# Performance work log

Hardware: AMD Instinct MI355X
Metric: run time of the kernel (lower is better)

Reference implementation:

```python
import jax, jax.numpy as jnp
import numpy as np

B, T, C, H, HD = 4, 2048, 1024, 16, 64

def setup_inputs() -> dict:
    key = jax.random.key(0)
    ks = jax.random.split(key, 9)
    s = 1.0 / np.sqrt(C)
    return {
        "x":  jax.random.normal(ks[0], (B, T, C), jnp.float32),
        "Wq": jax.random.normal(ks[1], (H, C, HD), jnp.float32) * s,
        "bq": jax.random.normal(ks[2], (H, HD), jnp.float32) * 0.02,
        "Wk": jax.random.normal(ks[3], (H, C, HD), jnp.float32) * s,
        "bk": jax.random.normal(ks[4], (H, HD), jnp.float32) * 0.02,
        "Wv": jax.random.normal(ks[5], (H, C, HD), jnp.float32) * s,
        "bv": jax.random.normal(ks[6], (H, HD), jnp.float32) * 0.02,
        "Wo": jax.random.normal(ks[7], (C, C), jnp.float32) * s,
        "bo": jax.random.normal(ks[8], (C,), jnp.float32) * 0.02,
    }

def reference(x, Wq, bq, Wk, bk, Wv, bv, Wo, bo):
    # Batched per-head linear projections: [B,T,C] x [H,C,D] -> [B,H,T,D]
    q = jnp.einsum('btc,hcd->bhtd', x, Wq) + bq[None, :, None, :]
    k = jnp.einsum('btc,hcd->bhtd', x, Wk) + bk[None, :, None, :]
    v = jnp.einsum('btc,hcd->bhtd', x, Wv) + bv[None, :, None, :]
    scale = 1.0 / jnp.sqrt(jnp.asarray(HD, q.dtype))
    scores = jnp.einsum('bhtd,bhsd->bhts', q, k) * scale  # [B,H,T,T]
    causal = jnp.tril(jnp.ones((T, T), dtype=bool))
    scores = jnp.where(causal[None, None, :, :], scores, -jnp.inf)
    attn = jax.nn.softmax(scores, axis=-1)
    out = jnp.einsum('bhts,bhsd->bhtd', attn, v)          # [B,H,T,D]
    concat = out.transpose(0, 2, 1, 3).reshape(B, T, C)   # concat heads
    return concat @ Wo + bo
```

## Files before the change

### kernel.cpp

```cpp
#include <hip/hip_runtime.h>
#include <stdint.h>

#define TSEQ 2048
#define NHEAD 16

typedef __attribute__((ext_vector_type(8))) short bf16x8;
typedef __attribute__((ext_vector_type(4))) short bf16x4;
typedef __attribute__((ext_vector_type(4))) float f32x4;

__device__ __forceinline__ unsigned short f2bf(float f) {
  union { float f; uint32_t u; } c;
  c.f = f;
  uint32_t u = c.u;
  u += 0x7fffu + ((u >> 16) & 1u);
  return (unsigned short)(u >> 16);
}

__device__ __forceinline__ float fexp2(float x) {
#if __has_builtin(__builtin_amdgcn_exp2f)
  return __builtin_amdgcn_exp2f(x);
#else
  return __builtin_exp2f(x);
#endif
}

using as3_void  = __attribute__((address_space(3))) void;
using as1_cvoid = const __attribute__((address_space(1))) void;

__device__ __forceinline__ void gld_lds16(const void* g, void* l) {
  __builtin_amdgcn_global_load_lds((as1_cvoid*)g, (as3_void*)l, 16, 0, 0);
}


__global__ void cast_x_kernel(const float4* __restrict__ x, unsigned short* __restrict__ xb) {
  int i = blockIdx.x * 256 + threadIdx.x;
  float4 v = x[i];
  int e = i * 4;
  int m = e >> 10, k = e & 1023;
  int ks = k ^ ((m & 7) << 3);
  ushort4 o;
  o.x = f2bf(v.x); o.y = f2bf(v.y); o.z = f2bf(v.z); o.w = f2bf(v.w);
  *(ushort4*)(xb + (size_t)m * 1024 + ks) = o;
}

__global__ void repack_wqkv(const float* __restrict__ Wq, const float* __restrict__ Wk,
                            const float* __restrict__ Wv, unsigned short* __restrict__ BT) {
  __shared__ unsigned short tile[64][72];
  const float* W = (blockIdx.z == 0) ? Wq : (blockIdx.z == 1) ? Wk : Wv;
  const int h = blockIdx.y;
  const int c0 = blockIdx.x * 64;
  const int t = threadIdx.x;
  const float* src = W + ((size_t)h * 1024 + c0) * 64;
#pragma unroll
  for (int p = 0; p < 16; ++p) {
    int idx = p * 256 + t;
    int cc = idx >> 6, d = idx & 63;
    tile[cc][d] = f2bf(src[(size_t)cc * 64 + d]);
  }
  __syncthreads();
  unsigned short* dst = BT + ((size_t)blockIdx.z * 1024 + (size_t)h * 64) * 1024 + c0;
#pragma unroll
  for (int p = 0; p < 16; ++p) {
    int idx = p * 256 + t;
    int d = idx >> 6, cc = idx & 63;
    dst[(size_t)d * 1024 + (cc ^ ((d & 7) << 3))] = tile[cc][d];
  }
}

__global__ void repack_wo(const float* __restrict__ Wo, unsigned short* __restrict__ WoT) {
  __shared__ unsigned short tile[64][72];
  const int k0 = blockIdx.x * 64;
  const int n0 = blockIdx.y * 64;
  const int t = threadIdx.x;
#pragma unroll
  for (int p = 0; p < 16; ++p) {
    int idx = p * 256 + t;
    int kk = idx >> 6, nn = idx & 63;
    tile[kk][nn] = f2bf(Wo[(size_t)(k0 + kk) * 1024 + n0 + nn]);
  }
  __syncthreads();
#pragma unroll
  for (int p = 0; p < 16; ++p) {
    int idx = p * 256 + t;
    int nn = idx >> 6, kk = idx & 63;
    WoT[(size_t)(n0 + nn) * 1024 + k0 + (kk ^ ((nn & 7) << 3))] = tile[kk][nn];
  }
}


template <int MODE>
__global__ __launch_bounds__(256) void gemm_bt(
    const unsigned short* __restrict__ A, const unsigned short* __restrict__ BTm,
    const float* __restrict__ bias0, const float* __restrict__ bias1,
    const float* __restrict__ bias2,
    unsigned short* __restrict__ qo, unsigned short* __restrict__ ko,
    unsigned short* __restrict__ vto, float* __restrict__ outf,
    int K, int N) {
  __shared__ __align__(16) char lds[65536];

  const int tid = threadIdx.x, lane = tid & 63, wv = tid >> 6;
  const int wr = wv >> 1, wc = wv & 1;
  const int g = lane >> 4, r = lane & 15;
  const int m0 = blockIdx.x * 128, n0 = blockIdx.y * 128;
  const int xr = (r & 7) << 4;

  f32x4 acc[4][4] = {};

  const int arow = tid >> 3;
  const int acol = (tid & 7) * 8;
  const unsigned short* Ab = A + (size_t)(m0 + arow) * K + acol;
  const unsigned short* Bb = BTm + (size_t)(n0 + arow) * K + acol;

#define GSTAGE(b, kel) do {                                                 \
    char* ab_ = lds + (b) * 32768 + wv * 1024;                              \
    _Pragma("unroll") for (int i = 0; i < 4; ++i) {                         \
      gld_lds16(Ab + (size_t)i * 32 * K + (kel), ab_ + i * 4096);           \
      gld_lds16(Bb + (size_t)i * 32 * K + (kel), ab_ + 16384 + i * 4096);   \
    } } while (0)

  const int NT = K >> 6;
  GSTAGE(0, 0);
  __syncthreads();

  for (int t = 0; t < NT; ++t) {
    const int cur = t & 1;
    if (t + 1 < NT) GSTAGE(cur ^ 1, (t + 1) << 6);
    const char* Ar = lds + cur * 32768;
    const char* Br = Ar + 16384;
#pragma unroll
    for (int kk = 0; kk < 2; ++kk) {
      bf16x8 af[4], bfv[4];
#pragma unroll
      for (int f = 0; f < 4; ++f) {
        af[f]  = *(const bf16x8*)(Ar + (wr * 64 + f * 16 + r) * 128 + ((kk * 64 + g * 16) ^ xr));
        bfv[f] = *(const bf16x8*)(Br + (wc * 64 + f * 16 + r) * 128 + ((kk * 64 + g * 16) ^ xr));
      }
#pragma unroll
      for (int fm = 0; fm < 4; ++fm)
#pragma unroll
        for (int fn = 0; fn < 4; ++fn)
          acc[fm][fn] = __builtin_amdgcn_mfma_f32_16x16x32_bf16(af[fm], bfv[fn], acc[fm][fn], 0, 0, 0);
    }
    __syncthreads();
  }
#undef GSTAGE

  if (MODE == 0) {
    const int which = n0 >> 10;
    const float* bias = (which == 0) ? bias0 : (which == 1) ? bias1 : bias2;
    const float sc = (which == 0) ? 0.18033688011112042f : 1.0f;
    const int b = m0 >> 11;
    const int t0 = m0 & 2047;
    unsigned short* ep = (unsigned short*)lds;

#pragma unroll
    for (int h = 0; h < 2; ++h) {
      const int head = ((n0 & 1023) + h * 64) >> 6;
      const size_t bhb = (size_t)(b * NHEAD + head) * 131072;
      __syncthreads();
      if (wc == h) {
        if (which == 2) {
#pragma unroll
          for (int fn = 0; fn < 4; ++fn) {
            const int d = fn * 16 + r;
            const float bvl = bias[head * 64 + d];
#pragma unroll
            for (int fm = 0; fm < 4; ++fm)
#pragma unroll
              for (int j = 0; j < 4; ++j) {
                const int t = wr * 64 + fm * 16 + 4 * g + j;
                ep[d * 136 + t] = f2bf(acc[fm][fn][j] + bvl);
              }
          }
        } else {
#pragma unroll
          for (int fn = 0; fn < 4; ++fn) {
            const int d = fn * 16 + r;
            const float bvl = bias[head * 64 + d];
#pragma unroll
            for (int fm = 0; fm < 4; ++fm)
#pragma unroll
              for (int j = 0; j < 4; ++j) {
                const int t = wr * 64 + fm * 16 + 4 * g + j;
                ep[t * 72 + d] = f2bf((acc[fm][fn][j] + bvl) * sc);
              }
          }
        }
      }
      __syncthreads();
      if (which == 2) {
#pragma unroll
        for (int p = 0; p < 4; ++p) {
          const int d = p * 16 + (tid >> 4);
          const int u = tid & 15;
          const int c = u >> 3;
          const int w = u & 7;
          const int kk = w >> 2, gg = w & 3;
          const int base_t = c * 64 + kk * 32 + 4 * gg;
          union { bf16x4 h4[2]; bf16x8 v8; } cc2;
          cc2.h4[0] = *(const bf16x4*)(ep + d * 136 + base_t);
          cc2.h4[1] = *(const bf16x4*)(ep + d * 136 + base_t + 16);
          const int q_base = w * 8;
          *(bf16x8*)(vto + bhb + (size_t)((t0 >> 6) + c) * 4096 + (size_t)d * 64 +
                     (q_base ^ ((d & 7) << 3))) = cc2.v8;
        }
      } else {
        unsigned short* qk = (which == 1) ? ko : qo;
#pragma unroll
        for (int p = 0; p < 4; ++p) {
          const int row = p * 32 + (tid >> 3);
          const int seg = tid & 7;
          const bf16x8 v8 = *(const bf16x8*)(ep + row * 72 + seg * 8);
          const int tt = t0 + row;
          int dbase = seg * 8;
          if (which == 1) dbase ^= (tt & 7) << 3;
          *(bf16x8*)(qk + bhb + (size_t)tt * 64 + dbase) = v8;
        }
      }
    }
  } else {
    float* epf = (float*)lds;
#pragma unroll
    for (int h = 0; h < 2; ++h) {
      __syncthreads();
      if (wc == h) {
#pragma unroll
        for (int fn = 0; fn < 4; ++fn) {
          const int n = n0 + h * 64 + fn * 16 + r;
          const float bvl = bias0[n];
#pragma unroll
          for (int fm = 0; fm < 4; ++fm)
#pragma unroll
            for (int j = 0; j < 4; ++j)
              epf[(wr * 64 + fm * 16 + 4 * g + j) * 68 + fn * 16 + r] = acc[fm][fn][j] + bvl;
        }
      }
      __syncthreads();
#pragma unroll
      for (int p = 0; p < 8; ++p) {
        const int row = p * 16 + (tid >> 4);
        const int seg = tid & 15;
        const f32x4 v4 = *(const f32x4*)(epf + row * 68 + seg * 4);
        *(f32x4*)(outf + (size_t)(m0 + row) * N + n0 + h * 64 + seg * 4) = v4;
      }
    }
  }
}


__global__ __launch_bounds__(256) void attn_fwd(const unsigned short* __restrict__ Qm,
                                                const unsigned short* __restrict__ Km,
                                                const unsigned short* __restrict__ Vtm,
                                                unsigned short* __restrict__ Om) {
  __shared__ __align__(16) unsigned short Ks[2][4096];
  __shared__ __align__(16) unsigned short Vs[2][4096];

  const int tid = threadIdx.x, lane = tid & 63, wv = tid >> 6;
  const int g = lane >> 4, r = lane & 15;
  const int bh = blockIdx.x & 63;
  const int qp = 15 - (blockIdx.x >> 6);

  const unsigned short* Qp = Qm + (size_t)bh * 131072;
  const unsigned short* Kp = Km + (size_t)bh * 131072;
  const unsigned short* Vp = Vtm + (size_t)bh * 131072;

  const int qb[2] = {qp * 128 + wv * 16, qp * 128 + 64 + wv * 16};

  bf16x8 qf[2][2];
#pragma unroll
  for (int mi = 0; mi < 2; ++mi)
#pragma unroll
    for (int h2 = 0; h2 < 2; ++h2)
      qf[mi][h2] = *(const bf16x8*)(Qp + (size_t)(qb[mi] + r) * 64 + h2 * 32 + g * 8);

  f32x4 oacc[2][4] = {};
  float m_[2] = {-__builtin_inff(), -__builtin_inff()};
  float l_[2] = {0.f, 0.f};

#define ASTAGE(buf, c) do {                                                      \
    const unsigned short* kg_ = Kp + (size_t)(c) * 4096;                         \
    const unsigned short* vg_ = Vp + (size_t)(c) * 4096;                         \
    const int o0_ = wv * 1024;                                                   \
    gld_lds16(kg_ + (o0_ >> 1) + lane * 8, (char*)Ks[buf] + o0_);                \
    gld_lds16(vg_ + (o0_ >> 1) + lane * 8, (char*)Vs[buf] + o0_);                \
    gld_lds16(kg_ + ((o0_ + 4096) >> 1) + lane * 8, (char*)Ks[buf] + o0_ + 4096);\
    gld_lds16(vg_ + ((o0_ + 4096) >> 1) + lane * 8, (char*)Vs[buf] + o0_ + 4096);\
  } while (0)

  const int nt = qp * 2 + 2;
  ASTAGE(0, 0);
  __syncthreads();

  for (int t = 0; t < nt; ++t) {
    const int cur = t & 1;
    if (t + 1 < nt) ASTAGE(cur ^ 1, t + 1);

    const char* KsT = (const char*)Ks[cur];
    const char* VsT = (const char*)Vs[cur];
    const int sw = (r & 7) << 4;
    bf16x8 kf[4][2], vf[4][2];
#pragma unroll
    for (int tt = 0; tt < 4; ++tt) {
      const int rowb = (tt * 16 + r) * 128;
#pragma unroll
      for (int kk = 0; kk < 2; ++kk) {
        const int cb = (kk * 64 + g * 16) ^ sw;
        kf[tt][kk] = *(const bf16x8*)(KsT + rowb + cb);
        vf[tt][kk] = *(const bf16x8*)(VsT + rowb + cb);
      }
    }

#pragma unroll
    for (int mi = 0; mi < 2; ++mi) {
      const int qbm = qb[mi];
      if (t * 64 > qbm + 15) continue;

      f32x4 sT[4];
      __builtin_amdgcn_s_setprio(1);
#pragma unroll
      for (int tt = 0; tt < 4; ++tt) {
        f32x4 a = {0.f, 0.f, 0.f, 0.f};
        a = __builtin_amdgcn_mfma_f32_16x16x32_bf16(kf[tt][0], qf[mi][0], a, 0, 0, 0);
        a = __builtin_amdgcn_mfma_f32_16x16x32_bf16(kf[tt][1], qf[mi][1], a, 0, 0, 0);
        sT[tt] = a;
      }
      __builtin_amdgcn_s_setprio(0);

      const int qg = qbm + r;
      if (t * 64 + 63 > qbm) {
#pragma unroll
        for (int tt = 0; tt < 4; ++tt)
#pragma unroll
          for (int j = 0; j < 4; ++j) {
            const int kv = t * 64 + tt * 16 + 4 * g + j;
            sT[tt][j] = (kv <= qg) ? sT[tt][j] : -__builtin_inff();
          }
      }

      float tm[4];
#pragma unroll
      for (int tt = 0; tt < 4; ++tt)
        tm[tt] = fmaxf(fmaxf(sT[tt][0], sT[tt][1]), fmaxf(sT[tt][2], sT[tt][3]));
      const float mx = fmaxf(fmaxf(tm[0], tm[1]), fmaxf(tm[2], tm[3]));

      float mcur = m_[mi];
      const bool norescale = __all(mx <= mcur + 4.0f);
      if (!norescale) {
        float rmx = mx;
        rmx = fmaxf(rmx, __shfl_xor(rmx, 16));
        rmx = fmaxf(rmx, __shfl_xor(rmx, 32));
        const float mnew = fmaxf(mcur, rmx);
        const float rs = fexp2(mcur - mnew);
        m_[mi] = mnew;
        mcur = mnew;
        l_[mi] *= rs;
        float rsb[4];
#pragma unroll
        for (int j = 0; j < 4; ++j) rsb[j] = __shfl(rs, 4 * g + j);
#pragma unroll
        for (int df = 0; df < 4; ++df)
#pragma unroll
          for (int j = 0; j < 4; ++j) oacc[mi][df][j] *= rsb[j];
      }

      float ts = 0.f;
#pragma unroll
      for (int tt = 0; tt < 4; ++tt)
#pragma unroll
        for (int j = 0; j < 4; ++j) {
          const float p = fexp2(sT[tt][j] - mcur);
          sT[tt][j] = p;
          ts += p;
        }
      l_[mi] += ts;

      union { uint32_t w[8]; bf16x8 v[2]; } pu;
#pragma unroll
      for (int tt = 0; tt < 4; ++tt) {
        asm("v_cvt_pk_bf16_f32 %0, %1, %2" : "=v"(pu.w[2 * tt])
            : "v"(sT[tt][0]), "v"(sT[tt][1]));
        asm("v_cvt_pk_bf16_f32 %0, %1, %2" : "=v"(pu.w[2 * tt + 1])
            : "v"(sT[tt][2]), "v"(sT[tt][3]));
      }

      __builtin_amdgcn_s_setprio(1);
#pragma unroll
      for (int kk = 0; kk < 2; ++kk)
#pragma unroll
        for (int df = 0; df < 4; ++df)
          oacc[mi][df] = __builtin_amdgcn_mfma_f32_16x16x32_bf16(pu.v[kk], vf[df][kk], oacc[mi][df], 0, 0, 0);
      __builtin_amdgcn_s_setprio(0);
    }
    __syncthreads();
  }
#undef ASTAGE

  const int b = bh >> 4, h = bh & 15;
#pragma unroll
  for (int mi = 0; mi < 2; ++mi) {
    float lt = l_[mi];
    lt += __shfl_xor(lt, 16);
    lt += __shfl_xor(lt, 32);
    float inv[4];
#pragma unroll
    for (int j = 0; j < 4; ++j) {
      const float lb = __shfl(lt, 4 * g + j);
      inv[j] = __builtin_amdgcn_rcpf(lb);
    }
#pragma unroll
    for (int df = 0; df < 4; ++df)
#pragma unroll
      for (int j = 0; j < 4; ++j) {
        const int trow = qb[mi] + 4 * g + j;
        const float ov = oacc[mi][df][j] * inv[j];
        const int col = (df * 16 + r) ^ ((trow & 7) << 3);
        Om[((size_t)(b * TSEQ + trow)) * 1024 + h * 64 + col] = f2bf(ov);
      }
  }
}


extern "C" void kernel_launch(void* const* d_in, const int* in_sizes, int n_in,
                              void* d_out, int out_size, void* d_ws, size_t ws_size,
                              hipStream_t stream) {
  const float* x  = (const float*)d_in[0];
  const float* Wq = (const float*)d_in[1];
  const float* bq = (const float*)d_in[2];
  const float* Wk = (const float*)d_in[3];
  const float* bk = (const float*)d_in[4];
  const float* Wv = (const float*)d_in[5];
  const float* bv = (const float*)d_in[6];
  const float* Wo = (const float*)d_in[7];
  const float* bo = (const float*)d_in[8];
  float* out = (float*)d_out;

  unsigned short* xb  = (unsigned short*)d_ws;
  unsigned short* btq = xb + (size_t)8192 * 1024;
  unsigned short* wot = btq + (size_t)3072 * 1024;
  unsigned short* qb  = wot + (size_t)1024 * 1024;
  unsigned short* kb  = qb + (size_t)64 * 2048 * 64;
  unsigned short* vtb = kb + (size_t)64 * 2048 * 64;

  cast_x_kernel<<<8192, 256, 0, stream>>>((const float4*)x, xb);
  repack_wqkv<<<dim3(16, 16, 3), 256, 0, stream>>>(Wq, Wk, Wv, btq);
  repack_wo<<<dim3(16, 16), 256, 0, stream>>>(Wo, wot);

  gemm_bt<0><<<dim3(64, 24), 256, 0, stream>>>(xb, btq, bq, bk, bv, qb, kb, vtb,
                                               nullptr, 1024, 3072);
  attn_fwd<<<1024, 256, 0, stream>>>(qb, kb, vtb, xb);
  gemm_bt<1><<<dim3(64, 8), 256, 0, stream>>>(xb, wot, bo, nullptr, nullptr,
                                              nullptr, nullptr, nullptr, out,
                                              1024, 1024);
}
```

Before: 177.6 us.

## Replace QKV projection GEMM with 256x256-tile, 8-wave pipelined kernel

```diff
diff --git a/kernel.cpp b/kernel.cpp
--- a/kernel.cpp
+++ b/kernel.cpp
@@ -30,6 +30,9 @@
 __device__ __forceinline__ void gld_lds16(const void* g, void* l) {
   __builtin_amdgcn_global_load_lds((as1_cvoid*)g, (as3_void*)l, 16, 0, 0);
 }
+
+#define LGKM0() do { asm volatile("s_waitcnt lgkmcnt(0)" ::: "memory"); \
+                     __builtin_amdgcn_sched_barrier(0); } while (0)
 
 
 __global__ void cast_x_kernel(const float4* __restrict__ x, unsigned short* __restrict__ xb) {
@@ -88,14 +91,162 @@
 }
 
 
-template <int MODE>
-__global__ __launch_bounds__(256) void gemm_bt(
+__global__ __launch_bounds__(512, 2) void gemm256(
     const unsigned short* __restrict__ A, const unsigned short* __restrict__ BTm,
     const float* __restrict__ bias0, const float* __restrict__ bias1,
     const float* __restrict__ bias2,
     unsigned short* __restrict__ qo, unsigned short* __restrict__ ko,
-    unsigned short* __restrict__ vto, float* __restrict__ outf,
-    int K, int N) {
+    unsigned short* __restrict__ vto) {
+  __shared__ __align__(16) char lds[131072];
+  constexpr int K = 1024, NT = 16;
+
+  const int tid = threadIdx.x, lane = tid & 63, w = tid >> 6;
+  const int wr = w >> 2, wc = w & 3;
+  const int g = lane >> 4, r = lane & 15;
+  const int bid = blockIdx.x;
+  const int bid2 = (bid & 7) * 48 + (bid >> 3);
+  const int bx = bid2 / 12, by = bid2 % 12;
+  const int m0 = bx * 256, n0 = by * 256;
+  const int xr = (r & 7) << 4;
+
+  const unsigned short* Ag = A + (size_t)m0 * K;
+  const unsigned short* Bg = BTm + (size_t)n0 * K;
+
+  f32x4 acc[8][4] = {};
+  bf16x8 a_[4][2], b_[2][2];
+
+#define STAGEH(op, hh, tt) do {                                                   \
+    const unsigned short* gp_ = (op) ? Bg : Ag;                                   \
+    char* lp_ = lds + (op) * 65536 + ((tt) & 1) * 32768 + (hh) * 16384 + w * 1024;\
+    gld_lds16(gp_ + (size_t)((hh) * 128 + (tid >> 3)) * K + (tt) * 64 + (tid & 7) * 8, lp_);          \
+    gld_lds16(gp_ + (size_t)((hh) * 128 + 64 + (tid >> 3)) * K + (tt) * 64 + (tid & 7) * 8, lp_ + 8192); \
+  } while (0)
+
+#define RDA(mp, q_) do { _Pragma("unroll") for (int ii = 0; ii < 4; ++ii) {       \
+    const char* p_ = lds + (q_) * 32768 + (wr * 16 + ((mp) * 4 + ii) * 32 + r) * 128; \
+    a_[ii][0] = *(const bf16x8*)(p_ + ((g * 16) ^ xr));                           \
+    a_[ii][1] = *(const bf16x8*)(p_ + ((64 + g * 16) ^ xr)); } } while (0)
+
+#define RDB(np, q_) do { _Pragma("unroll") for (int jj = 0; jj < 2; ++jj) {       \
+    const char* p_ = lds + 65536 + (q_) * 32768 + (wc * 16 + ((np) * 2 + jj) * 64 + r) * 128; \
+    b_[jj][0] = *(const bf16x8*)(p_ + ((g * 16) ^ xr));                           \
+    b_[jj][1] = *(const bf16x8*)(p_ + ((64 + g * 16) ^ xr)); } } while (0)
+
+#define MFMA16(mp, np) do {                                                       \
+    __builtin_amdgcn_s_setprio(1);                                                \
+    _Pragma("unroll") for (int ii = 0; ii < 4; ++ii)                              \
+    _Pragma("unroll") for (int jj = 0; jj < 2; ++jj) {                            \
+      f32x4& ac_ = acc[(mp) * 4 + ii][(np) * 2 + jj];                             \
+      ac_ = __builtin_amdgcn_mfma_f32_16x16x32_bf16(a_[ii][0], b_[jj][0], ac_, 0, 0, 0); \
+      ac_ = __builtin_amdgcn_mfma_f32_16x16x32_bf16(a_[ii][1], b_[jj][1], ac_, 0, 0, 0); \
+    }                                                                             \
+    __builtin_amdgcn_s_setprio(0);                                                \
+  } while (0)
+
+  STAGEH(0, 0, 0); STAGEH(1, 0, 0); STAGEH(1, 1, 0); STAGEH(0, 1, 0);
+  STAGEH(0, 0, 1); STAGEH(1, 0, 1);
+  asm volatile("s_waitcnt vmcnt(4)" ::: "memory");
+  __builtin_amdgcn_s_barrier();
+
+  for (int j = 0; j < NT; ++j) {
+    const int q = j & 1;
+    RDA(0, q); RDB(0, q);
+    if (j + 1 < NT) STAGEH(1, 1, j + 1);
+    __builtin_amdgcn_s_barrier();
+    LGKM0();
+    MFMA16(0, 0);
+    __builtin_amdgcn_s_barrier();
+    RDB(1, q);
+    if (j + 1 < NT) STAGEH(0, 1, j + 1);
+    __builtin_amdgcn_s_barrier();
+    LGKM0();
+    MFMA16(0, 1);
+    __builtin_amdgcn_s_barrier();
+    RDA(1, q); RDB(0, q);
+    if (j + 2 < NT) STAGEH(0, 0, j + 2);
+    __builtin_amdgcn_s_barrier();
+    LGKM0();
+    MFMA16(1, 0);
+    __builtin_amdgcn_s_barrier();
+    RDB(1, q);
+    if (j + 2 < NT) STAGEH(1, 0, j + 2);
+    __builtin_amdgcn_s_barrier();
+    LGKM0();
+    MFMA16(1, 1);
+    if (j >= NT - 2) { asm volatile("s_waitcnt vmcnt(0)" ::: "memory"); }
+    else             { asm volatile("s_waitcnt vmcnt(4)" ::: "memory"); }
+    __builtin_amdgcn_s_barrier();
+  }
+#undef STAGEH
+#undef RDA
+#undef RDB
+#undef MFMA16
+
+  const int which = n0 >> 10;
+  const float* bias = (which == 0) ? bias0 : (which == 1) ? bias1 : bias2;
+  const float sc = (which == 0) ? 0.18033688011112042f : 1.0f;
+  const int b = m0 >> 11;
+  const int t0 = m0 & 2047;
+  const int hb0 = (n0 & 1023) >> 6;
+  unsigned short* ep = (unsigned short*)lds;
+
+  for (int h = 0; h < 4; ++h) {
+    const int head = hb0 + h;
+    const size_t bhb = (size_t)(b * NHEAD + head) * 131072;
+    const float bvl = bias[head * 64 + wc * 16 + r];
+    __syncthreads();
+    if (which == 2) {
+#pragma unroll
+      for (int ii = 0; ii < 8; ++ii)
+#pragma unroll
+        for (int j = 0; j < 4; ++j) {
+          const int tin = wr * 16 + ii * 32 + 4 * g + j;
+          ep[(wc * 16 + r) * 264 + tin] = f2bf(acc[ii][h][j] + bvl);
+        }
+    } else {
+#pragma unroll
+      for (int ii = 0; ii < 8; ++ii)
+#pragma unroll
+        for (int j = 0; j < 4; ++j) {
+          const int tin = wr * 16 + ii * 32 + 4 * g + j;
+          ep[tin * 72 + wc * 16 + r] = f2bf((acc[ii][h][j] + bvl) * sc);
+        }
+    }
+    __syncthreads();
+    if (which == 2) {
+#pragma unroll
+      for (int p = 0; p < 4; ++p) {
+        const int idx = p * 512 + tid;
+        const int d = idx >> 5, rem = idx & 31;
+        const int c = rem >> 3, wq = rem & 7;
+        const int kk2 = wq >> 2, gg = wq & 3;
+        const int base_t = c * 64 + kk2 * 32 + gg * 4;
+        union { bf16x4 h4[2]; bf16x8 v8; } cc2;
+        cc2.h4[0] = *(const bf16x4*)(ep + d * 264 + base_t);
+        cc2.h4[1] = *(const bf16x4*)(ep + d * 264 + base_t + 16);
+        *(bf16x8*)(vto + bhb + (size_t)((t0 >> 6) + c) * 4096 + (size_t)d * 64 +
+                   ((wq * 8) ^ ((d & 7) << 3))) = cc2.v8;
+      }
+    } else {
+      unsigned short* qk = (which == 1) ? ko : qo;
+#pragma unroll
+      for (int p = 0; p < 4; ++p) {
+        const int row = p * 64 + (tid >> 3);
+        const int seg = tid & 7;
+        const bf16x8 v8 = *(const bf16x8*)(ep + row * 72 + seg * 8);
+        const int tt = t0 + row;
+        int dbase = seg * 8;
+        if (which == 1) dbase ^= (tt & 7) << 3;
+        *(bf16x8*)(qk + bhb + (size_t)tt * 64 + dbase) = v8;
+      }
+    }
+  }
+}
+
+
+__global__ __launch_bounds__(256) void gemm_oproj(
+    const unsigned short* __restrict__ A, const unsigned short* __restrict__ BTm,
+    const float* __restrict__ bias0, float* __restrict__ outf, int K, int N) {
   __shared__ __align__(16) char lds[65536];
 
   const int tid = threadIdx.x, lane = tid & 63, wv = tid >> 6;
@@ -145,104 +296,29 @@
   }
 #undef GSTAGE
 
-  if (MODE == 0) {
-    const int which = n0 >> 10;
-    const float* bias = (which == 0) ? bias0 : (which == 1) ? bias1 : bias2;
-    const float sc = (which == 0) ? 0.18033688011112042f : 1.0f;
-    const int b = m0 >> 11;
-    const int t0 = m0 & 2047;
-    unsigned short* ep = (unsigned short*)lds;
-
-#pragma unroll
-    for (int h = 0; h < 2; ++h) {
-      const int head = ((n0 & 1023) + h * 64) >> 6;
-      const size_t bhb = (size_t)(b * NHEAD + head) * 131072;
-      __syncthreads();
-      if (wc == h) {
-        if (which == 2) {
-#pragma unroll
-          for (int fn = 0; fn < 4; ++fn) {
-            const int d = fn * 16 + r;
-            const float bvl = bias[head * 64 + d];
-#pragma unroll
-            for (int fm = 0; fm < 4; ++fm)
-#pragma unroll
-              for (int j = 0; j < 4; ++j) {
-                const int t = wr * 64 + fm * 16 + 4 * g + j;
-                ep[d * 136 + t] = f2bf(acc[fm][fn][j] + bvl);
-              }
-          }
-        } else {
-#pragma unroll
-          for (int fn = 0; fn < 4; ++fn) {
-            const int d = fn * 16 + r;
-            const float bvl = bias[head * 64 + d];
-#pragma unroll
-            for (int fm = 0; fm < 4; ++fm)
-#pragma unroll
-              for (int j = 0; j < 4; ++j) {
-                const int t = wr * 64 + fm * 16 + 4 * g + j;
-                ep[t * 72 + d] = f2bf((acc[fm][fn][j] + bvl) * sc);
-              }
-          }
-        }
-      }
-      __syncthreads();
-      if (which == 2) {
-#pragma unroll
-        for (int p = 0; p < 4; ++p) {
-          const int d = p * 16 + (tid >> 4);
-          const int u = tid & 15;
-          const int c = u >> 3;
-          const int w = u & 7;
-          const int kk = w >> 2, gg = w & 3;
-          const int base_t = c * 64 + kk * 32 + 4 * gg;
-          union { bf16x4 h4[2]; bf16x8 v8; } cc2;
-          cc2.h4[0] = *(const bf16x4*)(ep + d * 136 + base_t);
-          cc2.h4[1] = *(const bf16x4*)(ep + d * 136 + base_t + 16);
-          const int q_base = w * 8;
-          *(bf16x8*)(vto + bhb + (size_t)((t0 >> 6) + c) * 4096 + (size_t)d * 64 +
-                     (q_base ^ ((d & 7) << 3))) = cc2.v8;
-        }
-      } else {
-        unsigned short* qk = (which == 1) ? ko : qo;
-#pragma unroll
-        for (int p = 0; p < 4; ++p) {
-          const int row = p * 32 + (tid >> 3);
-          const int seg = tid & 7;
-          const bf16x8 v8 = *(const bf16x8*)(ep + row * 72 + seg * 8);
-          const int tt = t0 + row;
-          int dbase = seg * 8;
-          if (which == 1) dbase ^= (tt & 7) << 3;
-          *(bf16x8*)(qk + bhb + (size_t)tt * 64 + dbase) = v8;
-        }
-      }
-    }
-  } else {
-    float* epf = (float*)lds;
-#pragma unroll
-    for (int h = 0; h < 2; ++h) {
-      __syncthreads();
-      if (wc == h) {
-#pragma unroll
-        for (int fn = 0; fn < 4; ++fn) {
-          const int n = n0 + h * 64 + fn * 16 + r;
-          const float bvl = bias0[n];
-#pragma unroll
-          for (int fm = 0; fm < 4; ++fm)
-#pragma unroll
-            for (int j = 0; j < 4; ++j)
-              epf[(wr * 64 + fm * 16 + 4 * g + j) * 68 + fn * 16 + r] = acc[fm][fn][j] + bvl;
-        }
-      }
-      __syncthreads();
-#pragma unroll
-      for (int p = 0; p < 8; ++p) {
-        const int row = p * 16 + (tid >> 4);
-        const int seg = tid & 15;
-        const f32x4 v4 = *(const f32x4*)(epf + row * 68 + seg * 4);
-        *(f32x4*)(outf + (size_t)(m0 + row) * N + n0 + h * 64 + seg * 4) = v4;
-      }
+  float* epf = (float*)lds;
+#pragma unroll
+  for (int h = 0; h < 2; ++h) {
+    __syncthreads();
+    if (wc == h) {
+#pragma unroll
+      for (int fn = 0; fn < 4; ++fn) {
+        const int n = n0 + h * 64 + fn * 16 + r;
+        const float bvl = bias0[n];
+#pragma unroll
+        for (int fm = 0; fm < 4; ++fm)
+#pragma unroll
+          for (int j = 0; j < 4; ++j)
+            epf[(wr * 64 + fm * 16 + 4 * g + j) * 68 + fn * 16 + r] = acc[fm][fn][j] + bvl;
+      }
+    }
+    __syncthreads();
+#pragma unroll
+    for (int p = 0; p < 8; ++p) {
+      const int row = p * 16 + (tid >> 4);
+      const int seg = tid & 15;
+      const f32x4 v4 = *(const f32x4*)(epf + row * 68 + seg * 4);
+      *(f32x4*)(outf + (size_t)(m0 + row) * N + n0 + h * 64 + seg * 4) = v4;
     }
   }
 }
@@ -445,10 +521,7 @@
   repack_wqkv<<<dim3(16, 16, 3), 256, 0, stream>>>(Wq, Wk, Wv, btq);
   repack_wo<<<dim3(16, 16), 256, 0, stream>>>(Wo, wot);
 
-  gemm_bt<0><<<dim3(64, 24), 256, 0, stream>>>(xb, btq, bq, bk, bv, qb, kb, vtb,
-                                               nullptr, 1024, 3072);
+  gemm256<<<384, 512, 0, stream>>>(xb, btq, bq, bk, bv, qb, kb, vtb);
   attn_fwd<<<1024, 256, 0, stream>>>(qb, kb, vtb, xb);
-  gemm_bt<1><<<dim3(64, 8), 256, 0, stream>>>(xb, wot, bo, nullptr, nullptr,
-                                              nullptr, nullptr, nullptr, out,
-                                              1024, 1024);
-}
+  gemm_oproj<<<dim3(64, 8), 256, 0, stream>>>(xb, wot, bo, out, 1024, 1024);
+}
```

Result: slower. 183.2 us (+3.1%).
